# Kernel optimization log

Hardware: AMD Instinct MI355X
Metric: run time of the kernel (lower is better)

## Reference

```python
import jax, jax.numpy as jnp
import numpy as np

N = 100000   # nodes
E = 1600000  # edges
DIN, DH, DOUT = 128, 64, 40
EPS = 1e-5


def setup_inputs() -> dict:
    key = jax.random.key(0)
    ks = jax.random.split(key, 16)
    glorot = lambda k, shp: jax.random.normal(k, shp, jnp.float32) / np.float32(np.sqrt(shp[0]))
    return {
        'x': jax.random.normal(ks[0], (N, DIN), jnp.float32),
        'edge_index': jax.random.randint(ks[1], (2, E), 0, N, jnp.int64),
        'W0': glorot(ks[2], (DIN, DH)), 'b0': jnp.zeros((DH,), jnp.float32),
        'W1': glorot(ks[3], (DH, DH)),  'b1': jnp.zeros((DH,), jnp.float32),
        'W2': glorot(ks[4], (DH, DH)),  'b2': jnp.zeros((DH,), jnp.float32),
        'ln0_g': jnp.ones((DH,), jnp.float32), 'ln0_b': jnp.zeros((DH,), jnp.float32),
        'ln1_g': jnp.ones((DH,), jnp.float32), 'ln1_b': jnp.zeros((DH,), jnp.float32),
        'mpW0': glorot(ks[5], (DH, DH)),  'mpb0': jnp.zeros((DH,), jnp.float32),
        'mpW1': glorot(ks[6], (DH, DOUT)), 'mpb1': jnp.zeros((DOUT,), jnp.float32),
    }


def _layernorm(h, g, b):
    mu = jnp.mean(h, axis=-1, keepdims=True)
    var = jnp.mean(jnp.square(h - mu), axis=-1, keepdims=True)
    return (h - mu) * jax.lax.rsqrt(var + EPS) * g + b


def _gcn_conv(x, src, dst, norm_e, self_w, W, b):
    # PyG GCNConv: h = x W; out = sum_{(s,d)} norm * h[s] scattered to d,
    # plus self-loop term, plus bias.  norm = d^{-1/2}[s] * d^{-1/2}[d] on A+I.
    h = x @ W                                        # [N, out]
    agg = jnp.zeros_like(h).at[dst].add(h[src] * norm_e[:, None])
    agg = agg + h * self_w[:, None]                  # self loops (i,i)
    return agg + b


def reference(x, edge_index, W0, b0, W1, b1, W2, b2,
              ln0_g, ln0_b, ln1_g, ln1_b, mpW0, mpb0, mpW1, mpb1):
    src, dst = edge_index[0], edge_index[1]
    # degree on A + I (count incoming edges at dst, +1 for self loop)
    deg = jnp.zeros((N,), jnp.float32).at[dst].add(1.0) + 1.0
    dinv = jax.lax.rsqrt(deg)
    norm_e = dinv[src] * dinv[dst]                   # per-edge weight [E]
    self_w = dinv * dinv                             # self-loop weight [N]

    h = x
    convs = [(W0, b0), (W1, b1), (W2, b2)]
    lns = [(ln0_g, ln0_b), (ln1_g, ln1_b)]
    for i, (W, b) in enumerate(convs):
        h = _gcn_conv(h, src, dst, norm_e, self_w, W, b)
        h = jax.nn.relu(h)
        # dropout: training=False -> identity
        if i != len(convs) - 1:
            g, bb = lns[i]
            h = _layernorm(h, g, bb)

    # post_mp: Linear -> Dropout(identity) -> Linear
    h = h @ mpW0 + mpb0
    return h @ mpW1 + mpb1
```

## Files before the change

### kernel.cpp

```cpp
#include <hip/hip_runtime.h>
#include <hip/hip_bf16.h>

#define NN 100000
#define EE 1600000
#define DOUT 40
#define LN_EPS 1e-5f
#define NBUCK 391
#define TILE 4096
#define TBLK 391
#define BCAP 8192

typedef __attribute__((ext_vector_type(8))) short short8;
typedef __attribute__((ext_vector_type(4))) float f32x4;

__device__ __forceinline__ float blo(unsigned u) { return __uint_as_float(u << 16); }
__device__ __forceinline__ float bhi(unsigned u) { return __uint_as_float(u & 0xffff0000u); }
__device__ __forceinline__ unsigned bpack(float lo, float hi) {
    unsigned a = __float_as_uint(lo);
    unsigned b = __float_as_uint(hi);
    a = (a + 0x7fffu + ((a >> 16) & 1u)) >> 16;
    b = (b + 0x7fffu + ((b >> 16) & 1u)) & 0xffff0000u;
    return (a & 0xffffu) | b;
}

__global__ __launch_bounds__(1024, 4) void bucket_k(
        const int* __restrict__ src, const int* __restrict__ dst,
        int* __restrict__ bucketCur, unsigned* __restrict__ bE,
        const float* __restrict__ W0, const float* __restrict__ W1,
        const float* __restrict__ W2,
        const float* __restrict__ mpW0, const float* __restrict__ mpb0,
        const float* __restrict__ mpW1, const float* __restrict__ mpb1,
        uint4* __restrict__ W0pk, uint4* __restrict__ W1pk,
        uint4* __restrict__ W2pk, uint4* __restrict__ Wfpk,
        float* __restrict__ bf) {
    __shared__ int cnt[8][NBUCK];
    __shared__ int basew[8][NBUCK];
    int tid = threadIdx.x;
    if (blockIdx.x == TBLK) {
        float* sWf = (float*)&basew[0][0];
        for (int i = tid; i < 64 * 48; i += 1024) {
            int k = i / 48, n = i % 48;
            float acc = 0.f;
            if (n < DOUT) {
                for (int j = 0; j < 64; ++j) acc = fmaf(mpW0[k * 64 + j], mpW1[j * DOUT + n], acc);
            }
            sWf[i] = acc;
        }
        for (int n = tid; n < 48; n += 1024) {
            float acc = 0.f;
            if (n < DOUT) {
                acc = mpb1[n];
                for (int j = 0; j < 64; ++j) acc = fmaf(mpb0[j], mpW1[j * DOUT + n], acc);
            }
            bf[n] = acc;
        }
        for (int i = tid; i < 1024; i += 1024) {
            int lane = i & 63, ct = i >> 6;
            int q = lane >> 4, ln = lane & 15;
            int c = ct >> 2, t = ct & 3;
            int row0 = c * 32 + q * 8, col = t * 16 + ln;
            uint4 u;
            u.x = bpack(W0[(row0 + 0) * 64 + col], W0[(row0 + 1) * 64 + col]);
            u.y = bpack(W0[(row0 + 2) * 64 + col], W0[(row0 + 3) * 64 + col]);
            u.z = bpack(W0[(row0 + 4) * 64 + col], W0[(row0 + 5) * 64 + col]);
            u.w = bpack(W0[(row0 + 6) * 64 + col], W0[(row0 + 7) * 64 + col]);
            W0pk[i] = u;
        }
        for (int i = tid; i < 512; i += 1024) {
            int lane = i & 63, ct = i >> 6;
            int q = lane >> 4, ln = lane & 15;
            int c = ct >> 2, t = ct & 3;
            int row0 = c * 32 + q * 8, col = t * 16 + ln;
            uint4 u;
            u.x = bpack(W1[(row0 + 0) * 64 + col], W1[(row0 + 1) * 64 + col]);
            u.y = bpack(W1[(row0 + 2) * 64 + col], W1[(row0 + 3) * 64 + col]);
            u.z = bpack(W1[(row0 + 4) * 64 + col], W1[(row0 + 5) * 64 + col]);
            u.w = bpack(W1[(row0 + 6) * 64 + col], W1[(row0 + 7) * 64 + col]);
            W1pk[i] = u;
            uint4 v;
            v.x = bpack(W2[(row0 + 0) * 64 + col], W2[(row0 + 1) * 64 + col]);
            v.y = bpack(W2[(row0 + 2) * 64 + col], W2[(row0 + 3) * 64 + col]);
            v.z = bpack(W2[(row0 + 4) * 64 + col], W2[(row0 + 5) * 64 + col]);
            v.w = bpack(W2[(row0 + 6) * 64 + col], W2[(row0 + 7) * 64 + col]);
            W2pk[i] = v;
        }
        __syncthreads();
        for (int i = tid; i < 384; i += 1024) {
            int lane = i & 63, ct = i >> 6;
            int q = lane >> 4, ln = lane & 15;
            int c = ct / 3, t = ct % 3;
            int row0 = c * 32 + q * 8, col = t * 16 + ln;
            uint4 u;
            u.x = bpack(sWf[(row0 + 0) * 48 + col], sWf[(row0 + 1) * 48 + col]);
            u.y = bpack(sWf[(row0 + 2) * 48 + col], sWf[(row0 + 3) * 48 + col]);
            u.z = bpack(sWf[(row0 + 4) * 48 + col], sWf[(row0 + 5) * 48 + col]);
            u.w = bpack(sWf[(row0 + 6) * 48 + col], sWf[(row0 + 7) * 48 + col]);
            Wfpk[i] = u;
        }
        return;
    }
    int hv = tid >> 7;
    for (int i = tid; i < 8 * NBUCK; i += 1024) ((int*)cnt)[i] = 0;
    __syncthreads();
    const int4* dst4 = (const int4*)dst;
    const int4* src4 = (const int4*)src;
    long i4 = (long)blockIdx.x * 1024 + tid;
    int4 dv = make_int4(-1, -1, -1, -1);
    int4 sv = make_int4(0, 0, 0, 0);
    if (i4 < EE / 4) { dv = dst4[i4]; sv = src4[i4]; }
    int d[4] = {dv.x, dv.y, dv.z, dv.w};
    int s[4] = {sv.x, sv.y, sv.z, sv.w};
#pragma unroll
    for (int i = 0; i < 4; ++i) {
        if (d[i] >= 0) atomicAdd(&cnt[hv][d[i] >> 8], 1);
    }
    __syncthreads();
    for (int b = tid; b < NBUCK; b += 1024) {
        int c[8];
        int tot = 0;
#pragma unroll
        for (int w = 0; w < 8; ++w) { c[w] = cnt[w][b]; tot += c[w]; }
        int base = tot ? atomicAdd(&bucketCur[b], tot) : 0;
        int run = b * BCAP + base;
#pragma unroll
        for (int w = 0; w < 8; ++w) { basew[w][b] = run; run += c[w]; cnt[w][b] = 0; }
    }
    __syncthreads();
#pragma unroll
    for (int i = 0; i < 4; ++i) {
        if (d[i] >= 0) {
            int b = d[i] >> 8;
            int pos = basew[hv][b] + atomicAdd(&cnt[hv][b], 1);
            bE[pos] = (unsigned)s[i] | ((unsigned)(d[i] & 255) << 24);
        }
    }
}

__global__ __launch_bounds__(1024, 4) void reorder2_k(const int* __restrict__ bucketCur,
                                                      const unsigned* __restrict__ bE,
                                                      int* __restrict__ csrSrc,
                                                      int* __restrict__ degI,
                                                      int* __restrict__ cursor,
                                                      float* __restrict__ dinv) {
    __shared__ int sScan[512];
    __shared__ int sHist[256];
    __shared__ int sPre[256];
    __shared__ int sStart[256];
    int tid = threadIdx.x;
    int b = blockIdx.x;
    if (tid < 512) sScan[tid] = (tid < NBUCK) ? bucketCur[tid] : 0;
    __syncthreads();
    for (int off = 1; off < 512; off <<= 1) {
        int t = (tid >= off && tid < 512) ? sScan[tid - off] : 0;
        __syncthreads();
        if (tid < 512) sScan[tid] += t;
        __syncthreads();
    }
    int bbase = (b == 0) ? 0 : sScan[b - 1];
    if (tid < 256) sHist[tid] = 0;
    __syncthreads();
    int start = b * BCAP;
    int ecnt = bucketCur[b];
    int nq = ecnt >> 2;
    const uint4* bE4 = (const uint4*)(bE + start);
    for (int i = tid; i < nq; i += 1024) {
        uint4 v = bE4[i];
        atomicAdd(&sHist[v.x >> 24], 1);
        atomicAdd(&sHist[v.y >> 24], 1);
        atomicAdd(&sHist[v.z >> 24], 1);
        atomicAdd(&sHist[v.w >> 24], 1);
    }
    for (int e = (nq << 2) + tid; e < ecnt; e += 1024) {
        atomicAdd(&sHist[bE[start + e] >> 24], 1);
    }
    __syncthreads();
    if (tid < 256) sPre[tid] = sHist[tid];
    __syncthreads();
    for (int off = 1; off < 256; off <<= 1) {
        int t = (tid >= off && tid < 256) ? sPre[tid - off] : 0;
        __syncthreads();
        if (tid < 256) sPre[tid] += t;
        __syncthreads();
    }
    if (tid < 256) {
        int h = sHist[tid];
        int excl = sPre[tid] - h;
        int st = bbase + excl;
        sStart[tid] = st;
        int nd = (b << 8) + tid;
        if (nd < NN) {
            degI[nd] = h;
            cursor[nd] = st;
            dinv[nd] = rsqrtf((float)h + 1.0f);
        }
    }
    __syncthreads();
    for (int i = tid; i < nq; i += 1024) {
        uint4 v = bE4[i];
        int p0 = atomicAdd(&sStart[v.x >> 24], 1);
        csrSrc[p0] = (int)(v.x & 0xFFFFFFu);
        int p1 = atomicAdd(&sStart[v.y >> 24], 1);
        csrSrc[p1] = (int)(v.y & 0xFFFFFFu);
        int p2 = atomicAdd(&sStart[v.z >> 24], 1);
        csrSrc[p2] = (int)(v.z & 0xFFFFFFu);
        int p3 = atomicAdd(&sStart[v.w >> 24], 1);
        csrSrc[p3] = (int)(v.w & 0xFFFFFFu);
    }
    for (int e = (nq << 2) + tid; e < ecnt; e += 1024) {
        unsigned v = bE[start + e];
        int pos = atomicAdd(&sStart[v >> 24], 1);
        csrSrc[pos] = (int)(v & 0xFFFFFFu);
    }
}

__global__ __launch_bounds__(256, 4) void gemm0(const float* __restrict__ X,
                                                const uint4* __restrict__ Wpk,
                                                const float* __restrict__ dinv,
                                                unsigned* __restrict__ H) {
    __shared__ float sD[64 * 65];
    int tid = threadIdx.x;
    int wv = tid >> 6, lane = tid & 63;
    int q = lane >> 4, ln = lane & 15;
    int base = blockIdx.x * 64;
    int node = base + wv * 16 + ln;
    bool ok = node < NN;
    short8 afrag[4];
#pragma unroll
    for (int c = 0; c < 4; ++c) {
        float4 f0 = make_float4(0.f, 0.f, 0.f, 0.f);
        float4 f1 = make_float4(0.f, 0.f, 0.f, 0.f);
        if (ok) {
            const float4* xp = (const float4*)(X + (long)node * 128 + c * 32 + q * 8);
            f0 = xp[0];
            f1 = xp[1];
        }
        uint4 u;
        u.x = bpack(f0.x, f0.y);
        u.y = bpack(f0.z, f0.w);
        u.z = bpack(f1.x, f1.y);
        u.w = bpack(f1.z, f1.w);
        afrag[c] = __builtin_bit_cast(short8, u);
    }
#pragma unroll
    for (int t = 0; t < 4; ++t) {
        f32x4 acc = {0.f, 0.f, 0.f, 0.f};
#pragma unroll
        for (int c = 0; c < 4; ++c) {
            short8 bfrag = __builtin_bit_cast(short8, Wpk[(c * 4 + t) * 64 + lane]);
            acc = __builtin_amdgcn_mfma_f32_16x16x32_bf16(afrag[c], bfrag, acc, 0, 0, 0);
        }
#pragma unroll
        for (int r = 0; r < 4; ++r)
            sD[(wv * 16 + q * 4 + r) * 65 + t * 16 + ln] = acc[r];
    }
    __syncthreads();
    for (int i = tid; i < 64 * 32; i += 256) {
        int row = i >> 5, c2 = i & 31;
        int nd = base + row;
        if (nd < NN) {
            float di = dinv[nd];
            float lo = sD[row * 65 + c2 * 2] * di;
            float hi = sD[row * 65 + c2 * 2 + 1] * di;
            H[nd * 32 + c2] = bpack(lo, hi);
        }
    }
}

__global__ __launch_bounds__(256, 4) void gemm_b(const uint4* __restrict__ Hin4,
                                                 const uint4* __restrict__ Wpk,
                                                 const float* __restrict__ dinv,
                                                 unsigned* __restrict__ H) {
    __shared__ float sD[64 * 65];
    int tid = threadIdx.x;
    int wv = tid >> 6, lane = tid & 63;
    int q = lane >> 4, ln = lane & 15;
    int base = blockIdx.x * 64;
    int node = base + wv * 16 + ln;
    bool ok = node < NN;
    short8 afrag[2];
    {
        uint4 u0 = make_uint4(0u, 0u, 0u, 0u), u1 = u0;
        if (ok) {
            u0 = Hin4[(unsigned)node * 8u + (unsigned)q];
            u1 = Hin4[(unsigned)node * 8u + 4u + (unsigned)q];
        }
        afrag[0] = __builtin_bit_cast(short8, u0);
        afrag[1] = __builtin_bit_cast(short8, u1);
    }
#pragma unroll
    for (int t = 0; t < 4; ++t) {
        f32x4 acc = {0.f, 0.f, 0.f, 0.f};
#pragma unroll
        for (int c = 0; c < 2; ++c) {
            short8 bfrag = __builtin_bit_cast(short8, Wpk[(c * 4 + t) * 64 + lane]);
            acc = __builtin_amdgcn_mfma_f32_16x16x32_bf16(afrag[c], bfrag, acc, 0, 0, 0);
        }
#pragma unroll
        for (int r = 0; r < 4; ++r)
            sD[(wv * 16 + q * 4 + r) * 65 + t * 16 + ln] = acc[r];
    }
    __syncthreads();
    for (int i = tid; i < 64 * 32; i += 256) {
        int row = i >> 5, c2 = i & 31;
        int nd = base + row;
        if (nd < NN) {
            float di = dinv[nd];
            float lo = sD[row * 65 + c2 * 2] * di;
            float hi = sD[row * 65 + c2 * 2 + 1] * di;
            H[nd * 32 + c2] = bpack(lo, hi);
        }
    }
}

__global__ __launch_bounds__(256, 4) void agg_k(
        const int* __restrict__ cursor, const int* __restrict__ degI,
        const int* __restrict__ csrSrc, const float* __restrict__ dinv,
        const uint2* __restrict__ H2, const float4* __restrict__ bias4,
        const float4* __restrict__ g4, const float4* __restrict__ beta4,
        uint2* __restrict__ OUT2, int doLN) {
    int tid = threadIdx.x;
    int w = tid >> 6, lane = tid & 63;
    int g = lane >> 4;
    unsigned f = (unsigned)(lane & 15);
    unsigned node = (unsigned)(blockIdx.x * 4 + w);
    int start = cursor[node];
    int deg = degI[node];
    int myIdx = 0;
    if (lane < deg) myIdx = csrSrc[(unsigned)(start + lane)];
    uint2 qs = H2[node * 16u + f];
    float di = dinv[node];
    float4 bb = bias4[f];
    float ax = 0.f, ay = 0.f, az = 0.f, aw = 0.f;
    float bx = 0.f, by = 0.f, bz = 0.f, bw = 0.f;
    uint2 qa[4];
#pragma unroll
    for (int r = 0; r < 4; ++r) {
        int e = r * 4 + g;
        unsigned s = (unsigned)__shfl(myIdx, e);
        qa[r] = make_uint2(0u, 0u);
        if (e < deg) qa[r] = H2[s * 16u + f];
    }
    if (deg <= 16) {
#pragma unroll
        for (int r = 0; r < 4; r += 2) {
            ax += blo(qa[r].x);     ay += bhi(qa[r].x);
            az += blo(qa[r].y);     aw += bhi(qa[r].y);
            bx += blo(qa[r + 1].x); by += bhi(qa[r + 1].x);
            bz += blo(qa[r + 1].y); bw += bhi(qa[r + 1].y);
        }
    } else {
        uint2 qb[4];
#pragma unroll
        for (int r = 0; r < 4; ++r) {
            int e = 16 + r * 4 + g;
            unsigned s = (unsigned)__shfl(myIdx, e);
            qb[r] = make_uint2(0u, 0u);
            if (e < deg) qb[r] = H2[s * 16u + f];
        }
#pragma unroll
        for (int r = 0; r < 4; r += 2) {
            ax += blo(qa[r].x);     ay += bhi(qa[r].x);
            az += blo(qa[r].y);     aw += bhi(qa[r].y);
            bx += blo(qa[r + 1].x); by += bhi(qa[r + 1].x);
            bz += blo(qa[r + 1].y); bw += bhi(qa[r + 1].y);
        }
#pragma unroll
        for (int r = 0; r < 4; r += 2) {
            ax += blo(qb[r].x);     ay += bhi(qb[r].x);
            az += blo(qb[r].y);     aw += bhi(qb[r].y);
            bx += blo(qb[r + 1].x); by += bhi(qb[r + 1].x);
            bz += blo(qb[r + 1].y); bw += bhi(qb[r + 1].y);
        }
        if (deg > 32) {
            int R2 = (deg + 3) >> 2;
            if (R2 > 16) R2 = 16;
            for (int r = 8; r < R2; ++r) {
                int e = r * 4 + g;
                unsigned s = (unsigned)__shfl(myIdx, e);
                uint2 qq = make_uint2(0u, 0u);
                if (e < deg) qq = H2[s * 16u + f];
                ax += blo(qq.x); ay += bhi(qq.x); az += blo(qq.y); aw += bhi(qq.y);
            }
            for (int ee = 64 + g; ee < deg; ee += 4) {
                uint2 qq = H2[(unsigned)csrSrc[(unsigned)(start + ee)] * 16u + f];
                ax += blo(qq.x); ay += bhi(qq.x); az += blo(qq.y); aw += bhi(qq.y);
            }
        }
    }
    ax += bx; ay += by; az += bz; aw += bw;
    ax += __shfl_xor(ax, 16); ay += __shfl_xor(ay, 16);
    az += __shfl_xor(az, 16); aw += __shfl_xor(aw, 16);
    ax += __shfl_xor(ax, 32); ay += __shfl_xor(ay, 32);
    az += __shfl_xor(az, 32); aw += __shfl_xor(aw, 32);
    float vx = fmaxf((ax + blo(qs.x)) * di + bb.x, 0.f);
    float vy = fmaxf((ay + bhi(qs.x)) * di + bb.y, 0.f);
    float vz = fmaxf((az + blo(qs.y)) * di + bb.z, 0.f);
    float vw = fmaxf((aw + bhi(qs.y)) * di + bb.w, 0.f);
    if (doLN) {
        float s = vx + vy + vz + vw;
        s += __shfl_xor(s, 1); s += __shfl_xor(s, 2);
        s += __shfl_xor(s, 4); s += __shfl_xor(s, 8);
        float mu = s * (1.f / 64.f);
        vx -= mu; vy -= mu; vz -= mu; vw -= mu;
        float vs = vx * vx + vy * vy + vz * vz + vw * vw;
        vs += __shfl_xor(vs, 1); vs += __shfl_xor(vs, 2);
        vs += __shfl_xor(vs, 4); vs += __shfl_xor(vs, 8);
        float inv = rsqrtf(vs * (1.f / 64.f) + LN_EPS);
        float4 gg = g4[f];
        float4 tt = beta4[f];
        vx = vx * inv * gg.x + tt.x;
        vy = vy * inv * gg.y + tt.y;
        vz = vz * inv * gg.z + tt.z;
        vw = vw * inv * gg.w + tt.w;
    }
    if (g == 0) OUT2[node * 16u + f] = make_uint2(bpack(vx, vy), bpack(vz, vw));
}

__global__ __launch_bounds__(256, 4) void mlp_mfma(const uint4* __restrict__ Hin4,
                                                   const uint4* __restrict__ Wfpk,
                                                   const float* __restrict__ bf,
                                                   float* __restrict__ OUT) {
    int tid = threadIdx.x;
    int wv = tid >> 6, lane = tid & 63;
    int q = lane >> 4, ln = lane & 15;
    int base = blockIdx.x * 64;
    int node = base + wv * 16 + ln;
    bool ok = node < NN;
    short8 afrag[2];
    {
        uint4 u0 = make_uint4(0u, 0u, 0u, 0u), u1 = u0;
        if (ok) {
            u0 = Hin4[(unsigned)node * 8u + (unsigned)q];
            u1 = Hin4[(unsigned)node * 8u + 4u + (unsigned)q];
        }
        afrag[0] = __builtin_bit_cast(short8, u0);
        afrag[1] = __builtin_bit_cast(short8, u1);
    }
#pragma unroll
    for (int t = 0; t < 3; ++t) {
        f32x4 acc = {0.f, 0.f, 0.f, 0.f};
#pragma unroll
        for (int c = 0; c < 2; ++c) {
            short8 bfrag = __builtin_bit_cast(short8, Wfpk[(c * 3 + t) * 64 + lane]);
            acc = __builtin_amdgcn_mfma_f32_16x16x32_bf16(afrag[c], bfrag, acc, 0, 0, 0);
        }
        int col = t * 16 + ln;
        if (col < DOUT) {
            float bv = bf[col];
#pragma unroll
            for (int r = 0; r < 4; ++r) {
                int nd = base + wv * 16 + q * 4 + r;
                if (nd < NN) OUT[(long)nd * DOUT + col] = acc[r] + bv;
            }
        }
    }
}

extern "C" void kernel_launch(void* const* d_in, const int* in_sizes, int n_in,
                              void* d_out, int out_size, void* d_ws, size_t ws_size,
                              hipStream_t stream) {
    const float* x    = (const float*)d_in[0];
    const int*   ei   = (const int*)d_in[1];
    const int*   srcI = ei;
    const int*   dstI = ei + EE;
    const float* W0   = (const float*)d_in[2];
    const float* b0   = (const float*)d_in[3];
    const float* W1   = (const float*)d_in[4];
    const float* b1   = (const float*)d_in[5];
    const float* W2   = (const float*)d_in[6];
    const float* b2   = (const float*)d_in[7];
    const float* ln0g = (const float*)d_in[8];
    const float* ln0b = (const float*)d_in[9];
    const float* ln1g = (const float*)d_in[10];
    const float* ln1b = (const float*)d_in[11];
    const float* mpW0 = (const float*)d_in[12];
    const float* mpb0 = (const float*)d_in[13];
    const float* mpW1 = (const float*)d_in[14];
    const float* mpb1 = (const float*)d_in[15];
    float* out = (float*)d_out;

    char* ws = (char*)d_ws;
    float*    dinv      = (float*)   (ws + 0);
    int*      degI      = (int*)     (ws + 512l * 1024);
    int*      cursor    = (int*)     (ws + 1024l * 1024);
    int*      bucketCur = (int*)     (ws + 1600l * 1024);
    uint4*    W0pk      = (uint4*)   (ws + 1792l * 1024);
    uint4*    W1pk      = (uint4*)   (ws + 1824l * 1024);
    uint4*    W2pk      = (uint4*)   (ws + 1856l * 1024);
    uint4*    Wfpk      = (uint4*)   (ws + 1888l * 1024);
    float*    bfv       = (float*)   (ws + 1920l * 1024);
    unsigned* bE        = (unsigned*)(ws + 2048l * 1024);
    int*      csrSrc    = (int*)     (ws + 15l * 1024 * 1024);
    unsigned* bufA      = (unsigned*)(ws + 22l * 1024 * 1024);
    unsigned* bufB      = (unsigned*)(ws + 36l * 1024 * 1024);

    const int aggBlocks  = NN / 4;
    const int gemmBlocks = (NN + 63) / 64;

    hipMemsetAsync(bucketCur, 0, NBUCK * sizeof(int), stream);
    bucket_k<<<TBLK + 1, 1024, 0, stream>>>(srcI, dstI, bucketCur, bE,
                                            W0, W1, W2, mpW0, mpb0, mpW1, mpb1,
                                            W0pk, W1pk, W2pk, Wfpk, bfv);
    reorder2_k<<<NBUCK, 1024, 0, stream>>>(bucketCur, bE, csrSrc, degI, cursor, dinv);

    gemm0<<<gemmBlocks, 256, 0, stream>>>(x, W0pk, dinv, bufA);
    agg_k<<<aggBlocks, 256, 0, stream>>>(cursor, degI, csrSrc, dinv, (const uint2*)bufA,
                                         (const float4*)b0, (const float4*)ln0g,
                                         (const float4*)ln0b, (uint2*)bufB, 1);
    gemm_b<<<gemmBlocks, 256, 0, stream>>>((const uint4*)bufB, W1pk, dinv, bufA);
    agg_k<<<aggBlocks, 256, 0, stream>>>(cursor, degI, csrSrc, dinv, (const uint2*)bufA,
                                         (const float4*)b1, (const float4*)ln1g,
                                         (const float4*)ln1b, (uint2*)bufB, 1);
    gemm_b<<<gemmBlocks, 256, 0, stream>>>((const uint4*)bufB, W2pk, dinv, bufA);
    agg_k<<<aggBlocks, 256, 0, stream>>>(cursor, degI, csrSrc, dinv, (const uint2*)bufA,
                                         (const float4*)b2, (const float4*)ln0g,
                                         (const float4*)ln0b, (uint2*)bufB, 0);
    mlp_mfma<<<gemmBlocks, 256, 0, stream>>>((const uint4*)bufB, Wfpk, bfv, out);
}
```

Measured before the change: 311.1 us.

## Fuse aggregation with following dense GEMM into one kernel per layer

Each aggregation kernel now also performs the next layer's 64x64 (or final 64x40) matmul on MFMA, staging 16 aggregated node rows in shared memory. Blocks grow to 1024 threads covering 16 nodes, one wave per node. This removes the separate gemm_b and mlp_mfma launches along with the intermediate buffer write and re-read between them. In exchange it adds two block-wide barriers per block, leaves most waves idle during the MFMA phase, and raises the block size, which may affect occupancy and latency hiding for the gather.

```diff
diff --git a/kernel.cpp b/kernel.cpp
--- a/kernel.cpp
+++ b/kernel.cpp
@@ -266,63 +266,21 @@
     }
 }
 
-__global__ __launch_bounds__(256, 4) void gemm_b(const uint4* __restrict__ Hin4,
-                                                 const uint4* __restrict__ Wpk,
-                                                 const float* __restrict__ dinv,
-                                                 unsigned* __restrict__ H) {
-    __shared__ float sD[64 * 65];
-    int tid = threadIdx.x;
-    int wv = tid >> 6, lane = tid & 63;
-    int q = lane >> 4, ln = lane & 15;
-    int base = blockIdx.x * 64;
-    int node = base + wv * 16 + ln;
-    bool ok = node < NN;
-    short8 afrag[2];
-    {
-        uint4 u0 = make_uint4(0u, 0u, 0u, 0u), u1 = u0;
-        if (ok) {
-            u0 = Hin4[(unsigned)node * 8u + (unsigned)q];
-            u1 = Hin4[(unsigned)node * 8u + 4u + (unsigned)q];
-        }
-        afrag[0] = __builtin_bit_cast(short8, u0);
-        afrag[1] = __builtin_bit_cast(short8, u1);
-    }
-#pragma unroll
-    for (int t = 0; t < 4; ++t) {
-        f32x4 acc = {0.f, 0.f, 0.f, 0.f};
-#pragma unroll
-        for (int c = 0; c < 2; ++c) {
-            short8 bfrag = __builtin_bit_cast(short8, Wpk[(c * 4 + t) * 64 + lane]);
-            acc = __builtin_amdgcn_mfma_f32_16x16x32_bf16(afrag[c], bfrag, acc, 0, 0, 0);
-        }
-#pragma unroll
-        for (int r = 0; r < 4; ++r)
-            sD[(wv * 16 + q * 4 + r) * 65 + t * 16 + ln] = acc[r];
-    }
-    __syncthreads();
-    for (int i = tid; i < 64 * 32; i += 256) {
-        int row = i >> 5, c2 = i & 31;
-        int nd = base + row;
-        if (nd < NN) {
-            float di = dinv[nd];
-            float lo = sD[row * 65 + c2 * 2] * di;
-            float hi = sD[row * 65 + c2 * 2 + 1] * di;
-            H[nd * 32 + c2] = bpack(lo, hi);
-        }
-    }
-}
-
-__global__ __launch_bounds__(256, 4) void agg_k(
+template <int DOLN, int FINAL>
+__global__ __launch_bounds__(1024, 8) void aggf_k(
         const int* __restrict__ cursor, const int* __restrict__ degI,
         const int* __restrict__ csrSrc, const float* __restrict__ dinv,
         const uint2* __restrict__ H2, const float4* __restrict__ bias4,
         const float4* __restrict__ g4, const float4* __restrict__ beta4,
-        uint2* __restrict__ OUT2, int doLN) {
+        const uint4* __restrict__ Wpk, const float* __restrict__ bfv,
+        unsigned* __restrict__ Hout, float* __restrict__ outF) {
+    __shared__ __align__(16) unsigned sH[16][36];
+    __shared__ float sD[16 * 65];
     int tid = threadIdx.x;
-    int w = tid >> 6, lane = tid & 63;
+    int wv = tid >> 6, lane = tid & 63;
     int g = lane >> 4;
     unsigned f = (unsigned)(lane & 15);
-    unsigned node = (unsigned)(blockIdx.x * 4 + w);
+    unsigned node = (unsigned)(blockIdx.x * 16 + wv);
     int start = cursor[node];
     int deg = degI[node];
     int myIdx = 0;
@@ -396,7 +354,7 @@
     float vy = fmaxf((ay + bhi(qs.x)) * di + bb.y, 0.f);
     float vz = fmaxf((az + blo(qs.y)) * di + bb.z, 0.f);
     float vw = fmaxf((aw + bhi(qs.y)) * di + bb.w, 0.f);
-    if (doLN) {
+    if (DOLN) {
         float s = vx + vy + vz + vw;
         s += __shfl_xor(s, 1); s += __shfl_xor(s, 2);
         s += __shfl_xor(s, 4); s += __shfl_xor(s, 8);
@@ -413,45 +371,39 @@
         vz = vz * inv * gg.z + tt.z;
         vw = vw * inv * gg.w + tt.w;
     }
-    if (g == 0) OUT2[node * 16u + f] = make_uint2(bpack(vx, vy), bpack(vz, vw));
-}
-
-__global__ __launch_bounds__(256, 4) void mlp_mfma(const uint4* __restrict__ Hin4,
-                                                   const uint4* __restrict__ Wfpk,
-                                                   const float* __restrict__ bf,
-                                                   float* __restrict__ OUT) {
-    int tid = threadIdx.x;
-    int wv = tid >> 6, lane = tid & 63;
-    int q = lane >> 4, ln = lane & 15;
-    int base = blockIdx.x * 64;
-    int node = base + wv * 16 + ln;
-    bool ok = node < NN;
-    short8 afrag[2];
-    {
-        uint4 u0 = make_uint4(0u, 0u, 0u, 0u), u1 = u0;
-        if (ok) {
-            u0 = Hin4[(unsigned)node * 8u + (unsigned)q];
-            u1 = Hin4[(unsigned)node * 8u + 4u + (unsigned)q];
-        }
-        afrag[0] = __builtin_bit_cast(short8, u0);
-        afrag[1] = __builtin_bit_cast(short8, u1);
-    }
-#pragma unroll
-    for (int t = 0; t < 3; ++t) {
+    if (g == 0) {
+        sH[wv][2 * f] = bpack(vx, vy);
+        sH[wv][2 * f + 1] = bpack(vz, vw);
+    }
+    __syncthreads();
+    constexpr int NT = FINAL ? 3 : 4;
+    if (wv < NT) {
+        int q = lane >> 4, ln = lane & 15;
+        short8 a0 = __builtin_bit_cast(short8, ((const uint4*)sH[ln])[q]);
+        short8 a1 = __builtin_bit_cast(short8, ((const uint4*)sH[ln])[4 + q]);
         f32x4 acc = {0.f, 0.f, 0.f, 0.f};
-#pragma unroll
-        for (int c = 0; c < 2; ++c) {
-            short8 bfrag = __builtin_bit_cast(short8, Wfpk[(c * 3 + t) * 64 + lane]);
-            acc = __builtin_amdgcn_mfma_f32_16x16x32_bf16(afrag[c], bfrag, acc, 0, 0, 0);
-        }
-        int col = t * 16 + ln;
-        if (col < DOUT) {
-            float bv = bf[col];
-#pragma unroll
-            for (int r = 0; r < 4; ++r) {
-                int nd = base + wv * 16 + q * 4 + r;
-                if (nd < NN) OUT[(long)nd * DOUT + col] = acc[r] + bv;
-            }
+        acc = __builtin_amdgcn_mfma_f32_16x16x32_bf16(
+            a0, __builtin_bit_cast(short8, Wpk[(0 * NT + wv) * 64 + lane]), acc, 0, 0, 0);
+        acc = __builtin_amdgcn_mfma_f32_16x16x32_bf16(
+            a1, __builtin_bit_cast(short8, Wpk[(1 * NT + wv) * 64 + lane]), acc, 0, 0, 0);
+#pragma unroll
+        for (int r = 0; r < 4; ++r)
+            sD[(q * 4 + r) * 65 + wv * 16 + ln] = acc[r];
+    }
+    __syncthreads();
+    if (FINAL) {
+        for (int i = tid; i < 16 * DOUT; i += 1024) {
+            int row = i / DOUT, col = i % DOUT;
+            unsigned nd = (unsigned)(blockIdx.x * 16 + row);
+            outF[nd * (unsigned)DOUT + col] = sD[row * 65 + col] + bfv[col];
+        }
+    } else {
+        for (int i = tid; i < 16 * 32; i += 1024) {
+            int row = i >> 5, c2 = i & 31;
+            unsigned nd = (unsigned)(blockIdx.x * 16 + row);
+            float dn = dinv[nd];
+            Hout[nd * 32u + c2] = bpack(sD[row * 65 + c2 * 2] * dn,
+                                        sD[row * 65 + c2 * 2 + 1] * dn);
         }
     }
 }
@@ -494,7 +446,7 @@
     unsigned* bufA      = (unsigned*)(ws + 22l * 1024 * 1024);
     unsigned* bufB      = (unsigned*)(ws + 36l * 1024 * 1024);
 
-    const int aggBlocks  = NN / 4;
+    const int aggBlocks  = NN / 16;
     const int gemmBlocks = (NN + 63) / 64;
 
     hipMemsetAsync(bucketCur, 0, NBUCK * sizeof(int), stream);
@@ -504,16 +456,16 @@
     reorder2_k<<<NBUCK, 1024, 0, stream>>>(bucketCur, bE, csrSrc, degI, cursor, dinv);
 
     gemm0<<<gemmBlocks, 256, 0, stream>>>(x, W0pk, dinv, bufA);
-    agg_k<<<aggBlocks, 256, 0, stream>>>(cursor, degI, csrSrc, dinv, (const uint2*)bufA,
-                                         (const float4*)b0, (const float4*)ln0g,
-                                         (const float4*)ln0b, (uint2*)bufB, 1);
-    gemm_b<<<gemmBlocks, 256, 0, stream>>>((const uint4*)bufB, W1pk, dinv, bufA);
-    agg_k<<<aggBlocks, 256, 0, stream>>>(cursor, degI, csrSrc, dinv, (const uint2*)bufA,
-                                         (const float4*)b1, (const float4*)ln1g,
-                                         (const float4*)ln1b, (uint2*)bufB, 1);
-    gemm_b<<<gemmBlocks, 256, 0, stream>>>((const uint4*)bufB, W2pk, dinv, bufA);
-    agg_k<<<aggBlocks, 256, 0, stream>>>(cursor, degI, csrSrc, dinv, (const uint2*)bufA,
-                                         (const float4*)b2, (const float4*)ln0g,
-                                         (const float4*)ln0b, (uint2*)bufB, 0);
-    mlp_mfma<<<gemmBlocks, 256, 0, stream>>>((const uint4*)bufB, Wfpk, bfv, out);
-}
+    aggf_k<1, 0><<<aggBlocks, 1024, 0, stream>>>(cursor, degI, csrSrc, dinv,
+                                                 (const uint2*)bufA, (const float4*)b0,
+                                                 (const float4*)ln0g, (const float4*)ln0b,
+                                                 W1pk, bfv, bufB, out);
+    aggf_k<1, 0><<<aggBlocks, 1024, 0, stream>>>(cursor, degI, csrSrc, dinv,
+                                                 (const uint2*)bufB, (const float4*)b1,
+                                                 (const float4*)ln1g, (const float4*)ln1b,
+                                                 W2pk, bfv, bufA, out);
+    aggf_k<0, 1><<<aggBlocks, 1024, 0, stream>>>(cursor, degI, csrSrc, dinv,
+                                                 (const uint2*)bufA, (const float4*)b2,
+                                                 (const float4*)ln0g, (const float4*)ln0b,
+                                                 Wfpk, bfv, bufB, out);
+}
```

New measurement: 307.9 us. About the same (-1.0%).
